# Performance work log

Measured on AMD Instinct MI355X. Metric: run time of the kernel, lower is better.

Reference implementation:

```python
import jax, jax.numpy as jnp
import numpy as np

B, SK, SQ, H, D, N = 4, 4096, 4096, 16, 64, 32


def setup_inputs() -> dict:
    key = jax.random.key(0)
    k1, k2, k3, k4, k5 = jax.random.split(key, 5)
    return {
        "key_in": jax.random.normal(k1, (B, SK, H), jnp.float32),
        "value": jax.random.normal(k2, (B, SK, H * D), jnp.float32),
        "query": jax.random.normal(k3, (B, SQ, H), jnp.float32),
        "real_amps": jax.random.normal(k4, (H, 1, 1, N), jnp.float32),
        "imag_amps": jax.random.normal(k5, (H, 1, 1, N), jnp.float32) * 0.1,
    }


def reference(key_in, value, query, real_amps, imag_amps):
    h, n = real_amps.shape[0], real_amps.shape[-1]
    b, sk, _ = key_in.shape
    sq = query.shape[1]
    d = value.shape[-1] // h
    # non-trainable freqs buffer: N points in [0, 1] scaled by N*pi
    freqs = (jnp.arange(n, dtype=key_in.dtype) / (n - 1)) * n * jnp.pi  # (N,)
    # reshape to per-head layout: scalar feature per head for q/k
    q = jnp.transpose(query, (2, 0, 1))[..., None]   # (h, b, sq, 1)
    k = jnp.transpose(key_in, (2, 0, 1))[..., None]  # (h, b, sk, 1)
    v = jnp.transpose(value.reshape(b, sk, h, d), (2, 0, 1, 3))  # (h, b, sk, d)
    qp = freqs * q  # (h, b, sq, N)
    kp = freqs * k  # (h, b, sk, N)
    sin_q, cos_q = jnp.sin(qp), jnp.cos(qp)
    sin_k, cos_k = jnp.sin(kp), jnp.cos(kp)
    # trig feature maps, width 4N
    trig_q = jnp.concatenate(
        [real_amps * cos_q, real_amps * sin_q, imag_amps * sin_q, -imag_amps * cos_q],
        axis=-1,
    )  # (h, b, sq, 4N)
    trig_k = jnp.concatenate([cos_k, sin_k, cos_k, sin_k], axis=-1)  # (h, b, sk, 4N)
    # linear attention: (K^T V) then Q (K^T V)
    kv = jnp.einsum('hbkf,hbkd->hbfd', trig_k, v)        # (h, b, 4N, d)
    out = jnp.einsum('hbqf,hbfd->hbqd', trig_q, kv)       # (h, b, sq, d)
    return jnp.transpose(out, (1, 2, 0, 3)).reshape(b, sq, h * d)
```

## Files before the change

kernel.cpp:

```cpp
#include <hip/hip_runtime.h>
#include <math.h>

#define SK 4096
#define SQ 4096
#define HH 16
#define DD 64
#define NN 32

typedef __attribute__((ext_vector_type(8))) short short8;
typedef __attribute__((ext_vector_type(4))) float floatx4;
typedef __attribute__((ext_vector_type(4))) unsigned short us4;

__device__ __forceinline__ float freq_of(int n) {
    return (float)n * (32.0f * (float)M_PI / 31.0f);
}

__device__ __forceinline__ unsigned short f2bf(float x) {
    unsigned u = __float_as_uint(x);
    u += 0x7FFFu + ((u >> 16) & 1u);
    return (unsigned short)(u >> 16);
}

template <int NC>
__global__ __launch_bounds__(256) void k1_partial(
    const float* __restrict__ key_in, const float* __restrict__ value,
    float* __restrict__ P)
{
    constexpr int KPC = SK / NC;
    constexpr int NB  = KPC / 64;
    const int chunk = blockIdx.x & (NC - 1);
    const int bh    = blockIdx.x / NC;
    const int b = bh >> 4, h = bh & 15;
    const int tid = threadIdx.x;
    const int w = tid >> 6, l = tid & 63;

    __shared__ unsigned short vtb[2][64 * 64];
    __shared__ float kt[KPC];

    const int k0 = chunk * KPC;
    const int g  = tid & 15;
    const int kq = tid >> 4;

    #pragma unroll
    for (int i = 0; i < KPC / 256; ++i)
        kt[tid + i * 256] = key_in[(size_t)(b * SK + k0 + tid + i * 256) * HH + h];

    const int fl = l & 15;
    const int qd = l >> 4;
    const int feat = w * 16 + fl;
    const float fn = freq_of(feat & 31);
    const bool use_sin = (w >= 2);

    floatx4 acc[4];
    #pragma unroll
    for (int dt = 0; dt < 4; ++dt) acc[dt] = (floatx4){0.f, 0.f, 0.f, 0.f};

    union F4 { float4 v; float f[4]; };
    F4 L[2][4];

    auto vload = [&](int bb, int p) {
        const int kb = k0 + bb * 64;
        #pragma unroll
        for (int jj = 0; jj < 4; ++jj)
            L[p][jj].v = *(const float4*)(value
                + (size_t)(b * SK + kb + jj * 16 + kq) * (HH * DD) + h * DD + g * 4);
    };

    auto vstore = [&](int p) {
        #pragma unroll
        for (int e = 0; e < 4; ++e) {
            const int d = g * 4 + e;
            union { us4 v; unsigned short u[4]; } px;
            #pragma unroll
            for (int jj = 0; jj < 4; ++jj)
                px.u[jj] = f2bf(L[p][jj].f[e]);
            *(us4*)&vtb[p][d * 64 + ((((kq >> 1) ^ (d & 7)) << 3) | ((kq & 1) << 2))]
                = px.v;
        }
    };

    vload(0, 0);
    #pragma unroll
    for (int bb = 0; bb < NB; ++bb) {
        const int p = bb & 1;
        if (bb + 1 < NB) vload(bb + 1, p ^ 1);
        vstore(p);
        __syncthreads();

        #pragma unroll
        for (int s = 0; s < 2; ++s) {
            const int cb = bb * 64 + s * 8 + qd * 2;
            float2 p0 = *(const float2*)&kt[cb];
            float2 p1 = *(const float2*)&kt[cb + 16];
            float2 p2 = *(const float2*)&kt[cb + 32];
            float2 p3 = *(const float2*)&kt[cb + 48];
            float kj[8] = {p0.x, p1.x, p2.x, p3.x, p0.y, p1.y, p2.y, p3.y};

            union { short8 v; unsigned short u[8]; } A;
            #pragma unroll
            for (int j = 0; j < 8; ++j) {
                float ang = fn * kj[j];
                A.u[j] = f2bf(use_sin ? __sinf(ang) : __cosf(ang));
            }

            #pragma unroll
            for (int dt = 0; dt < 4; ++dt) {
                const int d = dt * 16 + fl;
                short8 B = *(const short8*)
                    &vtb[p][d * 64 + ((((s << 2) | qd) ^ (d & 7)) << 3)];
                acc[dt] = __builtin_amdgcn_mfma_f32_16x16x32_bf16(
                    A.v, B, acc[dt], 0, 0, 0);
            }
        }
    }

    float* Pb = P + ((size_t)chunk * 64 + bh) * (2 * NN * DD);
    #pragma unroll
    for (int dt = 0; dt < 4; ++dt)
        #pragma unroll
        for (int r = 0; r < 4; ++r) {
            int frow = w * 16 + qd * 4 + r;
            Pb[frow * DD + dt * 16 + fl] = acc[dt][r];
        }
}

template <int NC>
__global__ __launch_bounds__(256) void k1_reduce(
    const float* __restrict__ P, float* __restrict__ CS)
{
    int gid = (blockIdx.x * 256 + threadIdx.x) * 4;
    float4 a = {0.f, 0.f, 0.f, 0.f};
    #pragma unroll
    for (int c = 0; c < NC; ++c) {
        float4 v = *(const float4*)&P[(size_t)c * (64 * 2 * NN * DD) + gid];
        a.x += v.x; a.y += v.y; a.z += v.z; a.w += v.w;
    }
    *(float4*)&CS[gid] = a;
}

__global__ __launch_bounds__(256) void k2_out(
    const float* __restrict__ query, const float* __restrict__ ramps,
    const float* __restrict__ iamps, const float* __restrict__ CS,
    float* __restrict__ out)
{
    const int bh = blockIdx.x >> 5;
    const int qc = blockIdx.x & 31;
    const int b = bh >> 4, h = bh & 15;
    const int qbase = qc * 128;
    const int tid = threadIdx.x;
    const int w = tid >> 6, l = tid & 63;

    __shared__ unsigned short cst[64 * 64];
    __shared__ float qv[128];

    {
        const float* CSb = CS + (size_t)bh * (2 * NN * DD);
        const int feat = tid >> 2, dbase = (tid & 3) * 16;
        const int fb = feat >> 3, f7 = feat & 7;
        #pragma unroll
        for (int i = 0; i < 4; ++i) {
            float4 v = *(const float4*)&CSb[feat * DD + dbase + i * 4];
            float vv[4] = {v.x, v.y, v.z, v.w};
            #pragma unroll
            for (int e = 0; e < 4; ++e) {
                int d = dbase + i * 4 + e;
                cst[d * 64 + ((fb ^ (d & 7)) << 3) + f7] = f2bf(vv[e]);
            }
        }
    }
    if (tid < 128)
        qv[tid] = query[(size_t)(b * SQ + qbase + tid) * HH + h];
    __syncthreads();

    const int fl = l & 15, qd = l >> 4;
    const int nb = qd * 8;
    float4 raA = *(const float4*)&ramps[h * NN + nb];
    float4 raB = *(const float4*)&ramps[h * NN + nb + 4];
    float4 iaA = *(const float4*)&iamps[h * NN + nb];
    float4 iaB = *(const float4*)&iamps[h * NN + nb + 4];
    float ra[8] = {raA.x, raA.y, raA.z, raA.w, raB.x, raB.y, raB.z, raB.w};
    float ia[8] = {iaA.x, iaA.y, iaA.z, iaA.w, iaB.x, iaB.y, iaB.z, iaB.w};

    union AB { short8 v; unsigned short u[8]; };
    AB A0[2], A1[2];
    #pragma unroll
    for (int hh = 0; hh < 2; ++hh) {
        const float qval = qv[hh * 64 + w * 16 + fl];
        #pragma unroll
        for (int j = 0; j < 8; ++j) {
            float s, c;
            __sincosf(freq_of(nb + j) * qval, &s, &c);
            A0[hh].u[j] = f2bf(ra[j] * c + ia[j] * s);
            A1[hh].u[j] = f2bf(ra[j] * s - ia[j] * c);
        }
    }

    floatx4 acc[2][4];
    #pragma unroll
    for (int hh = 0; hh < 2; ++hh)
        #pragma unroll
        for (int dt = 0; dt < 4; ++dt) acc[hh][dt] = (floatx4){0.f, 0.f, 0.f, 0.f};

    #pragma unroll
    for (int dt = 0; dt < 4; ++dt) {
        const int d = dt * 16 + fl;
        short8 B0 = *(const short8*)&cst[d * 64 + ((qd ^ (d & 7)) << 3)];
        short8 B1 = *(const short8*)&cst[d * 64 + (((4 + qd) ^ (d & 7)) << 3)];
        #pragma unroll
        for (int hh = 0; hh < 2; ++hh) {
            acc[hh][dt] = __builtin_amdgcn_mfma_f32_16x16x32_bf16(
                A0[hh].v, B0, acc[hh][dt], 0, 0, 0);
            acc[hh][dt] = __builtin_amdgcn_mfma_f32_16x16x32_bf16(
                A1[hh].v, B1, acc[hh][dt], 0, 0, 0);
        }
    }

    float* ob = out + ((size_t)(b * SQ + qbase) * HH + h) * DD;
    #pragma unroll
    for (int hh = 0; hh < 2; ++hh)
        #pragma unroll
        for (int dt = 0; dt < 4; ++dt)
            #pragma unroll
            for (int r = 0; r < 4; ++r) {
                int q = hh * 64 + w * 16 + qd * 4 + r;
                ob[(size_t)q * (HH * DD) + dt * 16 + fl] = acc[hh][dt][r];
            }
}

extern "C" void kernel_launch(void* const* d_in, const int* in_sizes, int n_in,
                              void* d_out, int out_size, void* d_ws, size_t ws_size,
                              hipStream_t stream) {
    const float* key_in = (const float*)d_in[0];
    const float* value  = (const float*)d_in[1];
    const float* query  = (const float*)d_in[2];
    const float* ramps  = (const float*)d_in[3];
    const float* iamps  = (const float*)d_in[4];
    float* out = (float*)d_out;

    const size_t CS_FLOATS  = 64 * 2 * NN * DD;
    const size_t P16_FLOATS = (size_t)16 * CS_FLOATS;
    const size_t need16 = (P16_FLOATS + CS_FLOATS) * sizeof(float);

    float* P = (float*)d_ws;

    if (ws_size >= need16) {
        float* CSp = P + P16_FLOATS;
        hipLaunchKernelGGL((k1_partial<16>), dim3(64 * 16), dim3(256), 0, stream,
                           key_in, value, P);
        hipLaunchKernelGGL((k1_reduce<16>), dim3(CS_FLOATS / 1024), dim3(256), 0, stream,
                           P, CSp);
        hipLaunchKernelGGL(k2_out, dim3(64 * 32), dim3(256), 0, stream,
                           query, ramps, iamps, CSp, out);
    } else {
        float* CSp = P + (size_t)8 * CS_FLOATS;
        hipLaunchKernelGGL((k1_partial<8>), dim3(64 * 8), dim3(256), 0, stream,
                           key_in, value, P);
        hipLaunchKernelGGL((k1_reduce<8>), dim3(CS_FLOATS / 1024), dim3(256), 0, stream,
                           P, CSp);
        hipLaunchKernelGGL(k2_out, dim3(64 * 32), dim3(256), 0, stream,
                           query, ramps, iamps, CSp, out);
    }
}
```

Baseline: 136.1 us.

## Fuse partial, reduce and output stages into one cooperative kernel with grid syncs

Replaces the three launches (partial K^T V, chunk reduction, output projection) with a single cooperative kernel of 1024 blocks that separates the phases with grid.sync(), reusing shared memory across them. The aim is to remove two kernel launch gaps and the tail effects between stages. In exchange, every block must stay resident for the whole kernel, which adds grid-wide barrier cost and fixes the occupancy at four blocks per CU. If the cooperative launch fails, it falls back to the old three-kernel path.

```diff
diff --git a/kernel.cpp b/kernel.cpp
--- a/kernel.cpp
+++ b/kernel.cpp
@@ -1,5 +1,8 @@
 #include <hip/hip_runtime.h>
+#include <hip/hip_cooperative_groups.h>
 #include <math.h>
+
+namespace cg = cooperative_groups;
 
 #define SK 4096
 #define SQ 4096
@@ -19,6 +22,211 @@
     unsigned u = __float_as_uint(x);
     u += 0x7FFFu + ((u >> 16) & 1u);
     return (unsigned short)(u >> 16);
+}
+
+static constexpr int FNC  = 16;
+static constexpr int FKPC = SK / FNC;
+static constexpr int FNB  = FKPC / 64;
+
+__global__ __launch_bounds__(256, 4) void fused(
+    const float* __restrict__ key_in, const float* __restrict__ value,
+    const float* __restrict__ query, const float* __restrict__ ramps,
+    const float* __restrict__ iamps, float* __restrict__ P,
+    float* __restrict__ CS, float* __restrict__ out)
+{
+    cg::grid_group grid = cg::this_grid();
+    const int bid = blockIdx.x;
+    const int tid = threadIdx.x;
+    const int w = tid >> 6, l = tid & 63;
+    const int fl = l & 15, qd = l >> 4;
+
+    __shared__ __align__(16) char smraw[2 * 64 * 64 * 2 + FKPC * 4];
+    unsigned short (*vtb)[64 * 64] = (unsigned short (*)[64 * 64])smraw;
+    float* kt = (float*)(smraw + 16384);
+    unsigned short* cst = (unsigned short*)smraw;
+    float* qv = (float*)(smraw + 8192);
+
+    {
+        const int chunk = bid & (FNC - 1);
+        const int bh    = bid / FNC;
+        const int b = bh >> 4, h = bh & 15;
+        const int k0 = chunk * FKPC;
+        const int g  = tid & 15;
+        const int kq = tid >> 4;
+
+        kt[tid] = key_in[(size_t)(b * SK + k0 + tid) * HH + h];
+
+        const int feat = w * 16 + fl;
+        const float fn = freq_of(feat & 31);
+        const bool use_sin = (w >= 2);
+
+        floatx4 acc[4];
+        #pragma unroll
+        for (int dt = 0; dt < 4; ++dt) acc[dt] = (floatx4){0.f, 0.f, 0.f, 0.f};
+
+        union F4 { float4 v; float f[4]; };
+        F4 L[2][4];
+
+        auto vload = [&](int bb, int p) {
+            const int kb = k0 + bb * 64;
+            #pragma unroll
+            for (int jj = 0; jj < 4; ++jj)
+                L[p][jj].v = *(const float4*)(value
+                    + (size_t)(b * SK + kb + jj * 16 + kq) * (HH * DD) + h * DD + g * 4);
+        };
+        auto vstore = [&](int p) {
+            #pragma unroll
+            for (int e = 0; e < 4; ++e) {
+                const int d = g * 4 + e;
+                union { us4 v; unsigned short u[4]; } px;
+                #pragma unroll
+                for (int jj = 0; jj < 4; ++jj)
+                    px.u[jj] = f2bf(L[p][jj].f[e]);
+                *(us4*)&vtb[p][d * 64 + ((((kq >> 1) ^ (d & 7)) << 3) | ((kq & 1) << 2))]
+                    = px.v;
+            }
+        };
+
+        vload(0, 0);
+        #pragma unroll
+        for (int bb = 0; bb < FNB; ++bb) {
+            const int p = bb & 1;
+            if (bb + 1 < FNB) vload(bb + 1, p ^ 1);
+            vstore(p);
+            __syncthreads();
+
+            #pragma unroll
+            for (int s = 0; s < 2; ++s) {
+                const int cb = bb * 64 + s * 8 + qd * 2;
+                float2 p0 = *(const float2*)&kt[cb];
+                float2 p1 = *(const float2*)&kt[cb + 16];
+                float2 p2 = *(const float2*)&kt[cb + 32];
+                float2 p3 = *(const float2*)&kt[cb + 48];
+                float kj[8] = {p0.x, p1.x, p2.x, p3.x, p0.y, p1.y, p2.y, p3.y};
+
+                union { short8 v; unsigned short u[8]; } A;
+                #pragma unroll
+                for (int j = 0; j < 8; ++j) {
+                    float ang = fn * kj[j];
+                    A.u[j] = f2bf(use_sin ? __sinf(ang) : __cosf(ang));
+                }
+
+                #pragma unroll
+                for (int dt = 0; dt < 4; ++dt) {
+                    const int d = dt * 16 + fl;
+                    short8 B = *(const short8*)
+                        &vtb[p][d * 64 + ((((s << 2) | qd) ^ (d & 7)) << 3)];
+                    acc[dt] = __builtin_amdgcn_mfma_f32_16x16x32_bf16(
+                        A.v, B, acc[dt], 0, 0, 0);
+                }
+            }
+        }
+
+        float* Pb = P + ((size_t)chunk * 64 + bh) * (2 * NN * DD);
+        #pragma unroll
+        for (int dt = 0; dt < 4; ++dt)
+            #pragma unroll
+            for (int r = 0; r < 4; ++r)
+                Pb[(w * 16 + qd * 4 + r) * DD + dt * 16 + fl] = acc[dt][r];
+    }
+
+    grid.sync();
+
+    {
+        const int gid = bid * 256 + tid;
+        float a = 0.f;
+        #pragma unroll
+        for (int c = 0; c < FNC; ++c)
+            a += P[(size_t)c * (64 * 2 * NN * DD) + gid];
+        CS[gid] = a;
+    }
+
+    grid.sync();
+
+    {
+        const int v0 = bid * 2;
+        const int bh = v0 >> 5;
+        const int b = bh >> 4, h = bh & 15;
+        const int Q0 = (v0 & 31) * 128;
+
+        {
+            const float* CSb = CS + (size_t)bh * (2 * NN * DD);
+            const int feat = tid >> 2, dbase = (tid & 3) * 16;
+            const int fb = feat >> 3, f7 = feat & 7;
+            #pragma unroll
+            for (int i = 0; i < 4; ++i) {
+                float4 v4 = *(const float4*)&CSb[feat * DD + dbase + i * 4];
+                float vv[4] = {v4.x, v4.y, v4.z, v4.w};
+                #pragma unroll
+                for (int e = 0; e < 4; ++e) {
+                    int d = dbase + i * 4 + e;
+                    cst[d * 64 + ((fb ^ (d & 7)) << 3) + f7] = f2bf(vv[e]);
+                }
+            }
+            qv[tid] = query[(size_t)(b * SQ + Q0 + tid) * HH + h];
+        }
+        __syncthreads();
+
+        const int nb = qd * 8;
+        float4 raA = *(const float4*)&ramps[h * NN + nb];
+        float4 raB = *(const float4*)&ramps[h * NN + nb + 4];
+        float4 iaA = *(const float4*)&iamps[h * NN + nb];
+        float4 iaB = *(const float4*)&iamps[h * NN + nb + 4];
+        float ra[8] = {raA.x, raA.y, raA.z, raA.w, raB.x, raB.y, raB.z, raB.w};
+        float ia[8] = {iaA.x, iaA.y, iaA.z, iaA.w, iaB.x, iaB.y, iaB.z, iaB.w};
+
+        short8 B0[4], B1[4];
+        #pragma unroll
+        for (int dt = 0; dt < 4; ++dt) {
+            const int d = dt * 16 + fl;
+            B0[dt] = *(const short8*)&cst[d * 64 + ((qd ^ (d & 7)) << 3)];
+            B1[dt] = *(const short8*)&cst[d * 64 + (((4 + qd) ^ (d & 7)) << 3)];
+        }
+
+        #pragma unroll
+        for (int qq = 0; qq < 2; ++qq) {
+            union AB { short8 v; unsigned short u[8]; };
+            AB A0[2], A1[2];
+            #pragma unroll
+            for (int hh = 0; hh < 2; ++hh) {
+                const float qval = qv[qq * 128 + hh * 64 + w * 16 + fl];
+                #pragma unroll
+                for (int j = 0; j < 8; ++j) {
+                    float s, c;
+                    __sincosf(freq_of(nb + j) * qval, &s, &c);
+                    A0[hh].u[j] = f2bf(ra[j] * c + ia[j] * s);
+                    A1[hh].u[j] = f2bf(ra[j] * s - ia[j] * c);
+                }
+            }
+            floatx4 acc[2][4];
+            #pragma unroll
+            for (int hh = 0; hh < 2; ++hh)
+                #pragma unroll
+                for (int dt = 0; dt < 4; ++dt)
+                    acc[hh][dt] = (floatx4){0.f, 0.f, 0.f, 0.f};
+
+            #pragma unroll
+            for (int dt = 0; dt < 4; ++dt)
+                #pragma unroll
+                for (int hh = 0; hh < 2; ++hh) {
+                    acc[hh][dt] = __builtin_amdgcn_mfma_f32_16x16x32_bf16(
+                        A0[hh].v, B0[dt], acc[hh][dt], 0, 0, 0);
+                    acc[hh][dt] = __builtin_amdgcn_mfma_f32_16x16x32_bf16(
+                        A1[hh].v, B1[dt], acc[hh][dt], 0, 0, 0);
+                }
+
+            float* ob = out + ((size_t)(b * SQ + Q0 + qq * 128) * HH + h) * DD;
+            #pragma unroll
+            for (int hh = 0; hh < 2; ++hh)
+                #pragma unroll
+                for (int dt = 0; dt < 4; ++dt)
+                    #pragma unroll
+                    for (int r = 0; r < 4; ++r) {
+                        int q = hh * 64 + w * 16 + qd * 4 + r;
+                        ob[(size_t)q * (HH * DD) + dt * 16 + fl] = acc[hh][dt][r];
+                    }
+        }
+    }
 }
 
 template <int NC>
@@ -65,7 +273,6 @@
             L[p][jj].v = *(const float4*)(value
                 + (size_t)(b * SK + kb + jj * 16 + kq) * (HH * DD) + h * DD + g * 4);
     };
-
     auto vstore = [&](int p) {
         #pragma unroll
         for (int e = 0; e < 4; ++e) {
@@ -118,10 +325,8 @@
     #pragma unroll
     for (int dt = 0; dt < 4; ++dt)
         #pragma unroll
-        for (int r = 0; r < 4; ++r) {
-            int frow = w * 16 + qd * 4 + r;
-            Pb[frow * DD + dt * 16 + fl] = acc[dt][r];
-        }
+        for (int r = 0; r < 4; ++r)
+            Pb[(w * 16 + qd * 4 + r) * DD + dt * 16 + fl] = acc[dt][r];
 }
 
 template <int NC>
@@ -245,6 +450,14 @@
 
     if (ws_size >= need16) {
         float* CSp = P + P16_FLOATS;
+        void* args[] = {(void*)&key_in, (void*)&value, (void*)&query,
+                        (void*)&ramps, (void*)&iamps,
+                        (void*)&P, (void*)&CSp, (void*)&out};
+        hipError_t e = hipLaunchCooperativeKernel(
+            (const void*)fused, dim3(1024), dim3(256), args, 0, stream);
+        if (e == hipSuccess) return;
+        (void)hipGetLastError();
+
         hipLaunchKernelGGL((k1_partial<16>), dim3(64 * 16), dim3(256), 0, stream,
                            key_in, value, P);
         hipLaunchKernelGGL((k1_reduce<16>), dim3(CS_FLOATS / 1024), dim3(256), 0, stream,
```

New measurement: 356.7 us. +162.2%, slower.

## Emit swizzled bf16 KV state from reduce and process 256 queries per block

Applied to the files above, without the earlier changes.

The reduce kernel now converts the summed K^T V state to bf16 and writes it in the swizzled shared-memory layout. The output kernel can then copy it into LDS with plain vector loads instead of converting fp32 per block. The output kernel also handles 256 queries per block in two passes, which halves the block count and the repeated state loads. In exchange there are fewer blocks for occupancy and the reduce kernel does scattered 2-byte stores.

```diff
diff --git a/kernel.cpp b/kernel.cpp
--- a/kernel.cpp
+++ b/kernel.cpp
@@ -65,7 +65,6 @@
             L[p][jj].v = *(const float4*)(value
                 + (size_t)(b * SK + kb + jj * 16 + kq) * (HH * DD) + h * DD + g * 4);
     };
-
     auto vstore = [&](int p) {
         #pragma unroll
         for (int e = 0; e < 4; ++e) {
@@ -118,61 +117,57 @@
     #pragma unroll
     for (int dt = 0; dt < 4; ++dt)
         #pragma unroll
-        for (int r = 0; r < 4; ++r) {
-            int frow = w * 16 + qd * 4 + r;
-            Pb[frow * DD + dt * 16 + fl] = acc[dt][r];
-        }
+        for (int r = 0; r < 4; ++r)
+            Pb[(w * 16 + qd * 4 + r) * DD + dt * 16 + fl] = acc[dt][r];
 }
 
 template <int NC>
-__global__ __launch_bounds__(256) void k1_reduce(
-    const float* __restrict__ P, float* __restrict__ CS)
+__global__ __launch_bounds__(256) void k1_reduce_bf16(
+    const float* __restrict__ P, unsigned short* __restrict__ CSb)
 {
-    int gid = (blockIdx.x * 256 + threadIdx.x) * 4;
+    const int gid4 = (blockIdx.x * 256 + threadIdx.x) * 4;
     float4 a = {0.f, 0.f, 0.f, 0.f};
     #pragma unroll
     for (int c = 0; c < NC; ++c) {
-        float4 v = *(const float4*)&P[(size_t)c * (64 * 2 * NN * DD) + gid];
+        float4 v = *(const float4*)&P[(size_t)c * (64 * 2 * NN * DD) + gid4];
         a.x += v.x; a.y += v.y; a.z += v.z; a.w += v.w;
     }
-    *(float4*)&CS[gid] = a;
+    const int bh = gid4 >> 12;
+    const int feat = (gid4 >> 6) & 63;
+    const int d0 = gid4 & 63;
+    const int fb = feat >> 3, f7 = feat & 7;
+    unsigned short* o = CSb + (size_t)bh * (2 * NN * DD);
+    float av[4] = {a.x, a.y, a.z, a.w};
+    #pragma unroll
+    for (int e = 0; e < 4; ++e) {
+        const int d = d0 + e;
+        o[d * 64 + ((fb ^ (d & 7)) << 3) + f7] = f2bf(av[e]);
+    }
 }
 
 __global__ __launch_bounds__(256) void k2_out(
     const float* __restrict__ query, const float* __restrict__ ramps,
-    const float* __restrict__ iamps, const float* __restrict__ CS,
+    const float* __restrict__ iamps, const unsigned short* __restrict__ CSb,
     float* __restrict__ out)
 {
-    const int bh = blockIdx.x >> 5;
-    const int qc = blockIdx.x & 31;
+    const int bh = blockIdx.x >> 4;
+    const int q0 = (blockIdx.x & 15) * 256;
     const int b = bh >> 4, h = bh & 15;
-    const int qbase = qc * 128;
     const int tid = threadIdx.x;
     const int w = tid >> 6, l = tid & 63;
+    const int fl = l & 15, qd = l >> 4;
 
     __shared__ unsigned short cst[64 * 64];
-    __shared__ float qv[128];
+    __shared__ float qv[256];
 
     {
-        const float* CSb = CS + (size_t)bh * (2 * NN * DD);
-        const int feat = tid >> 2, dbase = (tid & 3) * 16;
-        const int fb = feat >> 3, f7 = feat & 7;
-        #pragma unroll
-        for (int i = 0; i < 4; ++i) {
-            float4 v = *(const float4*)&CSb[feat * DD + dbase + i * 4];
-            float vv[4] = {v.x, v.y, v.z, v.w};
-            #pragma unroll
-            for (int e = 0; e < 4; ++e) {
-                int d = dbase + i * 4 + e;
-                cst[d * 64 + ((fb ^ (d & 7)) << 3) + f7] = f2bf(vv[e]);
-            }
-        }
-    }
-    if (tid < 128)
-        qv[tid] = query[(size_t)(b * SQ + qbase + tid) * HH + h];
+        const uint4* src = (const uint4*)(CSb + (size_t)bh * (2 * NN * DD));
+        *(uint4*)&cst[tid * 8]        = src[tid];
+        *(uint4*)&cst[2048 + tid * 8] = src[256 + tid];
+    }
+    qv[tid] = query[(size_t)(b * SQ + q0 + tid) * HH + h];
     __syncthreads();
 
-    const int fl = l & 15, qd = l >> 4;
     const int nb = qd * 8;
     float4 raA = *(const float4*)&ramps[h * NN + nb];
     float4 raB = *(const float4*)&ramps[h * NN + nb + 4];
@@ -181,50 +176,58 @@
     float ra[8] = {raA.x, raA.y, raA.z, raA.w, raB.x, raB.y, raB.z, raB.w};
     float ia[8] = {iaA.x, iaA.y, iaA.z, iaA.w, iaB.x, iaB.y, iaB.z, iaB.w};
 
-    union AB { short8 v; unsigned short u[8]; };
-    AB A0[2], A1[2];
-    #pragma unroll
-    for (int hh = 0; hh < 2; ++hh) {
-        const float qval = qv[hh * 64 + w * 16 + fl];
-        #pragma unroll
-        for (int j = 0; j < 8; ++j) {
-            float s, c;
-            __sincosf(freq_of(nb + j) * qval, &s, &c);
-            A0[hh].u[j] = f2bf(ra[j] * c + ia[j] * s);
-            A1[hh].u[j] = f2bf(ra[j] * s - ia[j] * c);
-        }
-    }
-
-    floatx4 acc[2][4];
-    #pragma unroll
-    for (int hh = 0; hh < 2; ++hh)
-        #pragma unroll
-        for (int dt = 0; dt < 4; ++dt) acc[hh][dt] = (floatx4){0.f, 0.f, 0.f, 0.f};
-
+    short8 B0[4], B1[4];
     #pragma unroll
     for (int dt = 0; dt < 4; ++dt) {
         const int d = dt * 16 + fl;
-        short8 B0 = *(const short8*)&cst[d * 64 + ((qd ^ (d & 7)) << 3)];
-        short8 B1 = *(const short8*)&cst[d * 64 + (((4 + qd) ^ (d & 7)) << 3)];
+        B0[dt] = *(const short8*)&cst[d * 64 + ((qd ^ (d & 7)) << 3)];
+        B1[dt] = *(const short8*)&cst[d * 64 + (((4 + qd) ^ (d & 7)) << 3)];
+    }
+
+    #pragma unroll
+    for (int qq = 0; qq < 2; ++qq) {
+        union AB { short8 v; unsigned short u[8]; };
+        AB A0[2], A1[2];
         #pragma unroll
         for (int hh = 0; hh < 2; ++hh) {
-            acc[hh][dt] = __builtin_amdgcn_mfma_f32_16x16x32_bf16(
-                A0[hh].v, B0, acc[hh][dt], 0, 0, 0);
-            acc[hh][dt] = __builtin_amdgcn_mfma_f32_16x16x32_bf16(
-                A1[hh].v, B1, acc[hh][dt], 0, 0, 0);
+            const float qval = qv[qq * 128 + hh * 64 + w * 16 + fl];
+            #pragma unroll
+            for (int j = 0; j < 8; ++j) {
+                float s, c;
+                __sincosf(freq_of(nb + j) * qval, &s, &c);
+                A0[hh].u[j] = f2bf(ra[j] * c + ia[j] * s);
+                A1[hh].u[j] = f2bf(ra[j] * s - ia[j] * c);
+            }
         }
-    }
-
-    float* ob = out + ((size_t)(b * SQ + qbase) * HH + h) * DD;
-    #pragma unroll
-    for (int hh = 0; hh < 2; ++hh)
+
+        floatx4 acc[2][4];
+        #pragma unroll
+        for (int hh = 0; hh < 2; ++hh)
+            #pragma unroll
+            for (int dt = 0; dt < 4; ++dt)
+                acc[hh][dt] = (floatx4){0.f, 0.f, 0.f, 0.f};
+
         #pragma unroll
         for (int dt = 0; dt < 4; ++dt)
             #pragma unroll
-            for (int r = 0; r < 4; ++r) {
-                int q = hh * 64 + w * 16 + qd * 4 + r;
-                ob[(size_t)q * (HH * DD) + dt * 16 + fl] = acc[hh][dt][r];
-            }
+            for (int hh = 0; hh < 2; ++hh) {
+                acc[hh][dt] = __builtin_amdgcn_mfma_f32_16x16x32_bf16(
+                    A0[hh].v, B0[dt], acc[hh][dt], 0, 0, 0);
+                acc[hh][dt] = __builtin_amdgcn_mfma_f32_16x16x32_bf16(
+                    A1[hh].v, B1[dt], acc[hh][dt], 0, 0, 0);
+            }
+
+        float* ob = out + ((size_t)(b * SQ + q0 + qq * 128) * HH + h) * DD;
+        #pragma unroll
+        for (int hh = 0; hh < 2; ++hh)
+            #pragma unroll
+            for (int dt = 0; dt < 4; ++dt)
+                #pragma unroll
+                for (int r = 0; r < 4; ++r) {
+                    int q = hh * 64 + w * 16 + qd * 4 + r;
+                    ob[(size_t)q * (HH * DD) + dt * 16 + fl] = acc[hh][dt][r];
+                }
+    }
 }
 
 extern "C" void kernel_launch(void* const* d_in, const int* in_sizes, int n_in,
@@ -239,25 +242,25 @@
 
     const size_t CS_FLOATS  = 64 * 2 * NN * DD;
     const size_t P16_FLOATS = (size_t)16 * CS_FLOATS;
-    const size_t need16 = (P16_FLOATS + CS_FLOATS) * sizeof(float);
+    const size_t need16 = P16_FLOATS * sizeof(float) + CS_FLOATS * sizeof(unsigned short);
 
     float* P = (float*)d_ws;
 
     if (ws_size >= need16) {
-        float* CSp = P + P16_FLOATS;
+        unsigned short* CSb = (unsigned short*)(P + P16_FLOATS);
         hipLaunchKernelGGL((k1_partial<16>), dim3(64 * 16), dim3(256), 0, stream,
                            key_in, value, P);
-        hipLaunchKernelGGL((k1_reduce<16>), dim3(CS_FLOATS / 1024), dim3(256), 0, stream,
-                           P, CSp);
-        hipLaunchKernelGGL(k2_out, dim3(64 * 32), dim3(256), 0, stream,
-                           query, ramps, iamps, CSp, out);
+        hipLaunchKernelGGL((k1_reduce_bf16<16>), dim3(CS_FLOATS / 1024), dim3(256), 0,
+                           stream, P, CSb);
+        hipLaunchKernelGGL(k2_out, dim3(64 * 16), dim3(256), 0, stream,
+                           query, ramps, iamps, CSb, out);
     } else {
-        float* CSp = P + (size_t)8 * CS_FLOATS;
+        unsigned short* CSb = (unsigned short*)(P + (size_t)8 * CS_FLOATS);
         hipLaunchKernelGGL((k1_partial<8>), dim3(64 * 8), dim3(256), 0, stream,
                            key_in, value, P);
-        hipLaunchKernelGGL((k1_reduce<8>), dim3(CS_FLOATS / 1024), dim3(256), 0, stream,
-                           P, CSp);
-        hipLaunchKernelGGL(k2_out, dim3(64 * 32), dim3(256), 0, stream,
-                           query, ramps, iamps, CSp, out);
-    }
-}
+        hipLaunchKernelGGL((k1_reduce_bf16<8>), dim3(CS_FLOATS / 1024), dim3(256), 0,
+                           stream, P, CSb);
+        hipLaunchKernelGGL(k2_out, dim3(64 * 16), dim3(256), 0, stream,
+                           query, ramps, iamps, CSb, out);
+    }
+}
```

Result: no change. 134.6 us (-1.1%).
